# Performance work log

Hardware: AMD Instinct MI355X
Metric: run time of the kernel (lower is better)

## Reference

```python
import jax, jax.numpy as jnp
import numpy as np

B, S, H = 2, 2048, 2048
INTER = 1024
N_ROUTED = 8
ZERO = 4
TOTAL = N_ROUTED + ZERO
TOP_K = 2
SCALE = 1.5


def setup_inputs() -> dict:
    key = jax.random.key(0)
    k0, k1, k2, k3, k4, k5 = jax.random.split(key, 6)
    w = 0.02  # weight init scale
    return {
        "hidden_states": jax.random.normal(k0, (B, S, H), jnp.float32),
        "classifier_w": jax.random.normal(k1, (TOTAL, H), jnp.float32) * w,
        "e_score_correction_bias": jax.random.normal(k2, (TOTAL,), jnp.float32) * w,
        "gate_w": jax.random.normal(k3, (N_ROUTED, INTER, H), jnp.float32) * w,
        "up_w": jax.random.normal(k4, (N_ROUTED, INTER, H), jnp.float32) * w,
        "down_w": jax.random.normal(k5, (N_ROUTED, H, INTER), jnp.float32) * w,
    }


def reference(hidden_states, classifier_w, e_score_correction_bias, gate_w, up_w, down_w):
    x = hidden_states  # [B,S,H]
    total = classifier_w.shape[0]
    n_routed = gate_w.shape[0]

    # --- Router: softmax over all experts, bias only for selection ---
    logits = jnp.einsum('bsh,eh->bse', x, classifier_w)          # [B,S,total]
    probs = jax.nn.softmax(logits, axis=-1)
    biased = probs + e_score_correction_bias
    _, idx = jax.lax.top_k(biased, TOP_K)                         # [B,S,K] int
    rw = jnp.take_along_axis(probs, idx, axis=-1) * SCALE         # unbiased probs as weights

    # Dense per-expert weight via one-hot combine (Equal+Mul+ReduceSum in original)
    w_full = jnp.sum(jax.nn.one_hot(idx, total, dtype=x.dtype) * rw[..., None], axis=-2)  # [B,S,total]

    # --- Compute ALL routed experts densely (matches original op graph) ---
    g = jnp.einsum('bsh,eih->bsei', x, gate_w)                    # [B,S,E,INTER]
    u = jnp.einsum('bsh,eih->bsei', x, up_w)
    act = jax.nn.silu(g) * u
    expert_out = jnp.einsum('bsei,ehi->bseh', act, down_w)        # [B,S,E,H]

    out = jnp.einsum('bse,bseh->bsh', w_full[..., :n_routed], expert_out)
    # Zero (identity) experts pass hidden_states through
    out = out + x * jnp.sum(w_full[..., n_routed:], axis=-1, keepdims=True)
    return out
```

## Files before the change

kernel.cpp:

```cpp
#include <hip/hip_runtime.h>
#include <cstdint>

#define T_TOKENS 4096
#define HDIM 2048
#define IDIM 1024
#define NEXP 8
#define NTOT 12
#define MAX_SLOTS 8320

typedef __bf16 bf16x8_t __attribute__((ext_vector_type(8)));
typedef float f32x4_t __attribute__((ext_vector_type(4)));
typedef unsigned short u16x8_t __attribute__((ext_vector_type(8)));

__device__ __forceinline__ unsigned short f2bf(float f) {
    unsigned int u = __builtin_bit_cast(unsigned int, f);
    u += 0x7fffu + ((u >> 16) & 1u);
    return (unsigned short)(u >> 16);
}
__device__ __forceinline__ float bfu2f(unsigned short u) {
    unsigned int v = ((unsigned int)u) << 16;
    return __builtin_bit_cast(float, v);
}
__device__ __forceinline__ void async16(const unsigned short* g, unsigned short* l) {
    __builtin_amdgcn_global_load_lds(
        (const unsigned int __attribute__((address_space(1)))*)g,
        (unsigned int __attribute__((address_space(3)))*)l,
        16, 0, 0);
}
__device__ __forceinline__ void cvt16(const float* src, unsigned short* dst) {
    f32x4_t f0 = ((const f32x4_t*)src)[0];
    f32x4_t f1 = ((const f32x4_t*)src)[1];
    f32x4_t f2 = ((const f32x4_t*)src)[2];
    f32x4_t f3 = ((const f32x4_t*)src)[3];
    u16x8_t a, b;
#pragma unroll
    for (int j = 0; j < 4; ++j) { a[j] = f2bf(f0[j]); a[4 + j] = f2bf(f1[j]); }
#pragma unroll
    for (int j = 0; j < 4; ++j) { b[j] = f2bf(f2[j]); b[4 + j] = f2bf(f3[j]); }
    ((u16x8_t*)dst)[0] = a;
    ((u16x8_t*)dst)[1] = b;
}

__global__ void init_kernel(int* __restrict__ meta) {
    int i = threadIdx.x;
    if (i < 32) meta[i] = 0;
}

__global__ void noop_kernel() {}

__global__ void router_kernel(const float* __restrict__ x,
                              const float* __restrict__ cw,
                              const float* __restrict__ bias,
                              int* __restrict__ counts,
                              int* __restrict__ tok_e,
                              float* __restrict__ tok_w,
                              float* __restrict__ zero_w) {
    const int token = blockIdx.x;
    const int ln = threadIdx.x;
    const float* xr = x + (size_t)token * HDIM;
    float acc[NTOT];
#pragma unroll
    for (int e = 0; e < NTOT; ++e) acc[e] = 0.f;
    for (int h0 = ln * 4; h0 < HDIM; h0 += 256) {
        f32x4_t xv = *(const f32x4_t*)(xr + h0);
#pragma unroll
        for (int e = 0; e < NTOT; ++e) {
            f32x4_t wv = *(const f32x4_t*)(cw + e * HDIM + h0);
            acc[e] += xv[0] * wv[0] + xv[1] * wv[1] + xv[2] * wv[2] + xv[3] * wv[3];
        }
    }
#pragma unroll
    for (int e = 0; e < NTOT; ++e) {
        float v = acc[e];
#pragma unroll
        for (int s = 32; s > 0; s >>= 1) v += __shfl_xor(v, s, 64);
        acc[e] = v;
    }
    if (ln == 0) {
        float mx = acc[0];
#pragma unroll
        for (int e = 1; e < NTOT; ++e) mx = fmaxf(mx, acc[e]);
        float p[NTOT];
        float sum = 0.f;
#pragma unroll
        for (int e = 0; e < NTOT; ++e) { p[e] = __expf(acc[e] - mx); sum += p[e]; }
        float inv = 1.f / sum;
#pragma unroll
        for (int e = 0; e < NTOT; ++e) p[e] *= inv;
        float b[NTOT];
#pragma unroll
        for (int e = 0; e < NTOT; ++e) b[e] = p[e] + bias[e];
        int i0 = 0; float v0 = b[0];
#pragma unroll
        for (int e = 1; e < NTOT; ++e) if (b[e] > v0) { v0 = b[e]; i0 = e; }
        int i1 = -1; float v1 = -3.0e38f;
#pragma unroll
        for (int e = 0; e < NTOT; ++e) if (e != i0 && b[e] > v1) { v1 = b[e]; i1 = e; }
        if (i1 < 0) i1 = (i0 == 0) ? 1 : 0;
        float w0 = p[i0] * 1.5f, w1 = p[i1] * 1.5f;
        tok_e[2 * token] = i0; tok_e[2 * token + 1] = i1;
        tok_w[2 * token] = w0; tok_w[2 * token + 1] = w1;
        float zw = 0.f;
        if (i0 >= NEXP) zw += w0; else atomicAdd(&counts[i0], 1);
        if (i1 >= NEXP) zw += w1; else atomicAdd(&counts[i1], 1);
        zero_w[token] = zw;
    }
}

__global__ void scan_kernel(const int* __restrict__ counts, int* __restrict__ offs) {
    if (threadIdx.x == 0 && blockIdx.x == 0) {
        int a = 0;
        for (int e = 0; e < NEXP; ++e) {
            offs[e] = a;
            int c = counts[e];
            if (c < 0) c = 0;
            if (c > T_TOKENS) c = T_TOKENS;
            a += c;
        }
        if (a > 2 * T_TOKENS) a = 2 * T_TOKENS;
        offs[NEXP] = a;
    }
}

__global__ void place_kernel(const int* __restrict__ tok_e, const float* __restrict__ tok_w,
                             const int* __restrict__ offs, int* __restrict__ fill,
                             int* __restrict__ token_list, float* __restrict__ slot_w,
                             int* __restrict__ map) {
    int token = blockIdx.x * blockDim.x + threadIdx.x;
    if (token >= T_TOKENS) return;
#pragma unroll
    for (int j = 0; j < 2; ++j) {
        int e = tok_e[2 * token + j];
        int m = -1;
        if (e >= 0 && e < NEXP) {
            int pos = atomicAdd(&fill[e], 1);
            int slot = offs[e] + pos;
            if (slot >= 0 && slot < 2 * T_TOKENS) {
                token_list[slot] = token;
                slot_w[slot] = tok_w[2 * token + j];
                m = slot;
            }
        }
        map[2 * token + j] = m;
    }
}

__launch_bounds__(256, 2)
__global__ void gemm1_kernel(const float* __restrict__ x,
                             const float* __restrict__ gate_w,
                             const float* __restrict__ up_w,
                             const int* __restrict__ offs,
                             const int* __restrict__ token_list,
                             const float* __restrict__ slot_w,
                             unsigned short* __restrict__ act) {
    const int e = blockIdx.z;
    const int off = offs[e];
    int Me = offs[e + 1] - off;
    if (Me < 0) Me = 0;
    if (Me > T_TOKENS) Me = T_TOKENS;
    const int m0 = blockIdx.y * 128;
    if (m0 >= Me) return;
    const int n0 = blockIdx.x * 128;

    __shared__ __align__(16) unsigned short As[128][32];
    __shared__ __align__(16) unsigned short Gs[128][32];
    __shared__ __align__(16) unsigned short Us[128][32];

    const int tid = threadIdx.x;
    const int srow = tid >> 1;
    const int shalf = (tid & 1) * 16;

    int tr = m0 + srow; if (tr >= Me) tr = Me - 1;
    int tok = token_list[off + tr];
    if (tok < 0 || tok >= T_TOKENS) tok = 0;
    const float* aA = x + (size_t)tok * HDIM + shalf;
    const float* aG = gate_w + (size_t)e * IDIM * HDIM + (size_t)(n0 + srow) * HDIM + shalf;
    const float* aU = up_w + (size_t)e * IDIM * HDIM + (size_t)(n0 + srow) * HDIM + shalf;
    unsigned short* lA = &As[srow][shalf];
    unsigned short* lG = &Gs[srow][shalf];
    unsigned short* lU = &Us[srow][shalf];

    const int wv = tid >> 6, ln = tid & 63;
    const int wm = wv & 1, wn = wv >> 1;
    const int fr = ln & 15;
    const int fk = (ln >> 4) * 8;

    f32x4_t accg[4][4] = {};
    f32x4_t accu[4][4] = {};

    for (int k0 = 0; k0 < HDIM; k0 += 32) {
        cvt16(aA + k0, lA);
        cvt16(aG + k0, lG);
        cvt16(aU + k0, lU);
        __syncthreads();
        bf16x8_t af[4], gf[4], uf[4];
#pragma unroll
        for (int t = 0; t < 4; ++t) {
            af[t] = *(const bf16x8_t*)&As[wm * 64 + t * 16 + fr][fk];
            gf[t] = *(const bf16x8_t*)&Gs[wn * 64 + t * 16 + fr][fk];
            uf[t] = *(const bf16x8_t*)&Us[wn * 64 + t * 16 + fr][fk];
        }
#pragma unroll
        for (int mt = 0; mt < 4; ++mt)
#pragma unroll
            for (int nt = 0; nt < 4; ++nt) {
                accg[mt][nt] = __builtin_amdgcn_mfma_f32_16x16x32_bf16(af[mt], gf[nt], accg[mt][nt], 0, 0, 0);
                accu[mt][nt] = __builtin_amdgcn_mfma_f32_16x16x32_bf16(af[mt], uf[nt], accu[mt][nt], 0, 0, 0);
            }
        __syncthreads();
    }

#pragma unroll
    for (int mt = 0; mt < 4; ++mt) {
#pragma unroll
        for (int r = 0; r < 4; ++r) {
            int rloc = wm * 64 + mt * 16 + (ln >> 4) * 4 + r;
            int grow = m0 + rloc;
            if (grow < Me) {
                float w = slot_w[off + grow];
                size_t rb = (size_t)(off + grow) * IDIM + n0;
#pragma unroll
                for (int nt = 0; nt < 4; ++nt) {
                    float g = accg[mt][nt][r];
                    float u = accu[mt][nt][r];
                    float s = g / (1.f + __expf(-g));
                    act[rb + wn * 64 + nt * 16 + fr] = f2bf(s * u * w);
                }
            }
        }
    }
}

__launch_bounds__(256, 2)
__global__ void gemm2_kernel(const unsigned short* __restrict__ act,
                             const float* __restrict__ dwn,
                             const int* __restrict__ offs,
                             unsigned short* __restrict__ dout) {
    const int e = blockIdx.z;
    const int off = offs[e];
    int Me = offs[e + 1] - off;
    if (Me < 0) Me = 0;
    if (Me > T_TOKENS) Me = T_TOKENS;
    const int m0 = blockIdx.y * 128;
    if (m0 >= Me) return;
    const int n0 = blockIdx.x * 128;

    __shared__ __align__(16) unsigned short As[128][32];
    __shared__ __align__(16) unsigned short Bs[128][32];

    const int tid = threadIdx.x;
    const int wv = tid >> 6, ln = tid & 63;

    const int sr0 = wv * 16 + (ln >> 2);
    const int sc = (ln & 3) * 8;
    int ar0 = off + m0 + sr0;      if (ar0 >= MAX_SLOTS) ar0 = MAX_SLOTS - 1;
    int ar1 = off + m0 + 64 + sr0; if (ar1 >= MAX_SLOTS) ar1 = MAX_SLOTS - 1;
    const unsigned short* aA0 = act + (size_t)ar0 * IDIM + sc;
    const unsigned short* aA1 = act + (size_t)ar1 * IDIM + sc;
    unsigned short* lA0 = &As[wv * 16][0];
    unsigned short* lA1 = &As[64 + wv * 16][0];

    const int srow = tid >> 1;
    const int shalf = (tid & 1) * 16;
    const float* aB = dwn + (size_t)e * HDIM * IDIM + (size_t)(n0 + srow) * IDIM + shalf;
    unsigned short* lB = &Bs[srow][shalf];

    const int wm = wv & 1, wn = wv >> 1;
    const int fr = ln & 15;
    const int fk = (ln >> 4) * 8;

    f32x4_t acc[4][4] = {};

    for (int k0 = 0; k0 < IDIM; k0 += 32) {
        async16(aA0 + k0, lA0);
        async16(aA1 + k0, lA1);
        cvt16(aB + k0, lB);
        __syncthreads();
        bf16x8_t af[4], bfr[4];
#pragma unroll
        for (int t = 0; t < 4; ++t) {
            af[t] = *(const bf16x8_t*)&As[wm * 64 + t * 16 + fr][fk];
            bfr[t] = *(const bf16x8_t*)&Bs[wn * 64 + t * 16 + fr][fk];
        }
#pragma unroll
        for (int mt = 0; mt < 4; ++mt)
#pragma unroll
            for (int nt = 0; nt < 4; ++nt)
                acc[mt][nt] = __builtin_amdgcn_mfma_f32_16x16x32_bf16(af[mt], bfr[nt], acc[mt][nt], 0, 0, 0);
        __syncthreads();
    }

#pragma unroll
    for (int mt = 0; mt < 4; ++mt) {
#pragma unroll
        for (int r = 0; r < 4; ++r) {
            int rloc = wm * 64 + mt * 16 + (ln >> 4) * 4 + r;
            int grow = m0 + rloc;
            if (grow < Me) {
                size_t rb = (size_t)(off + grow) * HDIM + n0;
#pragma unroll
                for (int nt = 0; nt < 4; ++nt)
                    dout[rb + wn * 64 + nt * 16 + fr] = f2bf(acc[mt][nt][r]);
            }
        }
    }
}

__global__ void finalize_kernel(const float* __restrict__ x,
                                const unsigned short* __restrict__ dout,
                                const int* __restrict__ map,
                                const float* __restrict__ zero_w,
                                float* __restrict__ out) {
    int gid = blockIdx.x * blockDim.x + threadIdx.x;
    int token = gid >> 8;
    int hg = (gid & 255) * 8;
    int s0 = map[2 * token], s1 = map[2 * token + 1];
    float zw = zero_w[token];
    size_t base = (size_t)token * HDIM + hg;
    f32x4_t x0 = *(const f32x4_t*)(x + base);
    f32x4_t x1 = *(const f32x4_t*)(x + base + 4);
    float o[8];
#pragma unroll
    for (int j = 0; j < 4; ++j) { o[j] = zw * x0[j]; o[4 + j] = zw * x1[j]; }
    if (s0 >= 0 && s0 < 2 * T_TOKENS) {
        u16x8_t d = *(const u16x8_t*)(dout + (size_t)s0 * HDIM + hg);
#pragma unroll
        for (int j = 0; j < 8; ++j) o[j] += bfu2f(d[j]);
    }
    if (s1 >= 0 && s1 < 2 * T_TOKENS) {
        u16x8_t d = *(const u16x8_t*)(dout + (size_t)s1 * HDIM + hg);
#pragma unroll
        for (int j = 0; j < 8; ++j) o[j] += bfu2f(d[j]);
    }
    f32x4_t o0, o1;
#pragma unroll
    for (int j = 0; j < 4; ++j) { o0[j] = o[j]; o1[j] = o[4 + j]; }
    *(f32x4_t*)(out + base) = o0;
    *(f32x4_t*)(out + base + 4) = o1;
}

extern "C" void kernel_launch(void* const* d_in, const int* in_sizes, int n_in,
                              void* d_out, int out_size, void* d_ws, size_t ws_size,
                              hipStream_t stream) {
    const float* x = (const float*)d_in[0];
    const float* cw = (const float*)d_in[1];
    const float* bias = (const float*)d_in[2];
    const float* gw = (const float*)d_in[3];
    const float* uw = (const float*)d_in[4];
    const float* dw = (const float*)d_in[5];
    float* out = (float*)d_out;

    char* ws = (char*)d_ws;
    int* counts = (int*)(ws + 0);
    int* fill = (int*)(ws + 32);
    int* offs = (int*)(ws + 64);
    int* tok_e = (int*)(ws + 128);
    float* tok_w = (float*)(ws + 32896);
    float* zero_w = (float*)(ws + 65664);
    int* map = (int*)(ws + 82048);
    int* token_list = (int*)(ws + 114816);
    float* slot_w = (float*)(ws + 148096);
    unsigned short* act = (unsigned short*)(ws + 181504);
    unsigned short* dout = (unsigned short*)(ws + 181504 + 17039360);
    const size_t needed = 181504ull + 17039360ull + 34078720ull;
    if (ws_size < needed) {
        noop_kernel<<<1, 64, 0, stream>>>();
        return;
    }

    init_kernel<<<1, 64, 0, stream>>>((int*)ws);

    router_kernel<<<T_TOKENS, 64, 0, stream>>>(x, cw, bias, counts, tok_e, tok_w, zero_w);
    scan_kernel<<<1, 64, 0, stream>>>(counts, offs);
    place_kernel<<<(T_TOKENS + 255) / 256, 256, 0, stream>>>(tok_e, tok_w, offs, fill,
                                                             token_list, slot_w, map);
    gemm1_kernel<<<dim3(IDIM / 128, 32, NEXP), 256, 0, stream>>>(x, gw, uw, offs,
                                                                 token_list, slot_w, act);
    gemm2_kernel<<<dim3(HDIM / 128, 32, NEXP), 256, 0, stream>>>(act, dw, offs, dout);
    finalize_kernel<<<(T_TOKENS * HDIM / 8 + 255) / 256, 256, 0, stream>>>(x, dout, map,
                                                                           zero_w, out);
}
```

Baseline: 518.5 us.

## Pre-convert weights and activations to bf16 and use async LDS loads in GEMMs

Adds per-call kernels converting gate/up/down weights to bf16 in workspace and writes a bf16 copy of x from the router. GEMM kernels then load bf16 operands directly into LDS via global_load_lds, with gemm1 using 64-row tiles and higher occupancy. This removes in-loop fp32→bf16 conversion and halves repeated weight traffic, at the cost of an extra ~300MB conversion pass every call. A fallback keeps the old kernels when the workspace is too small.

```diff
diff --git a/kernel.cpp b/kernel.cpp
--- a/kernel.cpp
+++ b/kernel.cpp
@@ -11,6 +11,7 @@
 typedef __bf16 bf16x8_t __attribute__((ext_vector_type(8)));
 typedef float f32x4_t __attribute__((ext_vector_type(4)));
 typedef unsigned short u16x8_t __attribute__((ext_vector_type(8)));
+typedef unsigned short u16x4_t __attribute__((ext_vector_type(4)));
 
 __device__ __forceinline__ unsigned short f2bf(float f) {
     unsigned int u = __builtin_bit_cast(unsigned int, f);
@@ -48,13 +49,26 @@
 
 __global__ void noop_kernel() {}
 
+__global__ void cvtbf_kernel(const float* __restrict__ s, unsigned short* __restrict__ d, int n8) {
+    int stride = gridDim.x * blockDim.x;
+    for (int i = blockIdx.x * blockDim.x + threadIdx.x; i < n8; i += stride) {
+        const f32x4_t* p = (const f32x4_t*)(s + (size_t)i * 8);
+        f32x4_t a = p[0], b = p[1];
+        u16x8_t o;
+#pragma unroll
+        for (int j = 0; j < 4; ++j) { o[j] = f2bf(a[j]); o[4 + j] = f2bf(b[j]); }
+        ((u16x8_t*)d)[i] = o;
+    }
+}
+
 __global__ void router_kernel(const float* __restrict__ x,
                               const float* __restrict__ cw,
                               const float* __restrict__ bias,
                               int* __restrict__ counts,
                               int* __restrict__ tok_e,
                               float* __restrict__ tok_w,
-                              float* __restrict__ zero_w) {
+                              float* __restrict__ zero_w,
+                              unsigned short* __restrict__ xb) {
     const int token = blockIdx.x;
     const int ln = threadIdx.x;
     const float* xr = x + (size_t)token * HDIM;
@@ -63,6 +77,12 @@
     for (int e = 0; e < NTOT; ++e) acc[e] = 0.f;
     for (int h0 = ln * 4; h0 < HDIM; h0 += 256) {
         f32x4_t xv = *(const f32x4_t*)(xr + h0);
+        if (xb) {
+            u16x4_t o;
+#pragma unroll
+            for (int j = 0; j < 4; ++j) o[j] = f2bf(xv[j]);
+            *(u16x4_t*)(xb + (size_t)token * HDIM + h0) = o;
+        }
 #pragma unroll
         for (int e = 0; e < NTOT; ++e) {
             f32x4_t wv = *(const f32x4_t*)(cw + e * HDIM + h0);
@@ -145,10 +165,10 @@
     }
 }
 
-__launch_bounds__(256, 2)
-__global__ void gemm1_kernel(const float* __restrict__ x,
-                             const float* __restrict__ gate_w,
-                             const float* __restrict__ up_w,
+__launch_bounds__(256, 3)
+__global__ void gemm1_kernel(const unsigned short* __restrict__ xb,
+                             const unsigned short* __restrict__ gwb,
+                             const unsigned short* __restrict__ uwb,
                              const int* __restrict__ offs,
                              const int* __restrict__ token_list,
                              const float* __restrict__ slot_w,
@@ -158,6 +178,178 @@
     int Me = offs[e + 1] - off;
     if (Me < 0) Me = 0;
     if (Me > T_TOKENS) Me = T_TOKENS;
+    const int m0 = blockIdx.y * 64;
+    if (m0 >= Me) return;
+    const int n0 = blockIdx.x * 128;
+
+    __shared__ __align__(16) unsigned short As[64][32];
+    __shared__ __align__(16) unsigned short Gs[128][32];
+    __shared__ __align__(16) unsigned short Us[128][32];
+
+    const int tid = threadIdx.x;
+    const int wv = tid >> 6, ln = tid & 63;
+
+    int tr = m0 + wv * 16 + (ln >> 2);
+    if (tr >= Me) tr = Me - 1;
+    int tok = token_list[off + tr];
+    if (tok < 0 || tok >= T_TOKENS) tok = 0;
+    const unsigned short* aA = xb + (size_t)tok * HDIM + (ln & 3) * 8;
+    unsigned short* lA = &As[wv * 16][0];
+
+    const size_t wrow = (size_t)(n0 + wv * 32 + (ln >> 2)) * HDIM + (ln & 3) * 8;
+    const unsigned short* aG0 = gwb + (size_t)e * IDIM * HDIM + wrow;
+    const unsigned short* aG1 = aG0 + (size_t)16 * HDIM;
+    const unsigned short* aU0 = uwb + (size_t)e * IDIM * HDIM + wrow;
+    const unsigned short* aU1 = aU0 + (size_t)16 * HDIM;
+    unsigned short* lG0 = &Gs[wv * 32][0];
+    unsigned short* lG1 = &Gs[wv * 32 + 16][0];
+    unsigned short* lU0 = &Us[wv * 32][0];
+    unsigned short* lU1 = &Us[wv * 32 + 16][0];
+
+    const int wm = wv & 1, wn = wv >> 1;
+    const int fr = ln & 15;
+    const int fk = (ln >> 4) * 8;
+
+    f32x4_t accg[2][4] = {};
+    f32x4_t accu[2][4] = {};
+
+    for (int k0 = 0; k0 < HDIM; k0 += 32) {
+        async16(aA + k0, lA);
+        async16(aG0 + k0, lG0);
+        async16(aG1 + k0, lG1);
+        async16(aU0 + k0, lU0);
+        async16(aU1 + k0, lU1);
+        __syncthreads();
+        bf16x8_t af[2], gf[4], uf[4];
+#pragma unroll
+        for (int t = 0; t < 2; ++t)
+            af[t] = *(const bf16x8_t*)&As[wm * 32 + t * 16 + fr][fk];
+#pragma unroll
+        for (int t = 0; t < 4; ++t) {
+            gf[t] = *(const bf16x8_t*)&Gs[wn * 64 + t * 16 + fr][fk];
+            uf[t] = *(const bf16x8_t*)&Us[wn * 64 + t * 16 + fr][fk];
+        }
+#pragma unroll
+        for (int mt = 0; mt < 2; ++mt)
+#pragma unroll
+            for (int nt = 0; nt < 4; ++nt) {
+                accg[mt][nt] = __builtin_amdgcn_mfma_f32_16x16x32_bf16(af[mt], gf[nt], accg[mt][nt], 0, 0, 0);
+                accu[mt][nt] = __builtin_amdgcn_mfma_f32_16x16x32_bf16(af[mt], uf[nt], accu[mt][nt], 0, 0, 0);
+            }
+        __syncthreads();
+    }
+
+#pragma unroll
+    for (int mt = 0; mt < 2; ++mt) {
+#pragma unroll
+        for (int r = 0; r < 4; ++r) {
+            int rloc = wm * 32 + mt * 16 + (ln >> 4) * 4 + r;
+            int grow = m0 + rloc;
+            if (grow < Me) {
+                float w = slot_w[off + grow];
+                size_t rb = (size_t)(off + grow) * IDIM + n0;
+#pragma unroll
+                for (int nt = 0; nt < 4; ++nt) {
+                    float g = accg[mt][nt][r];
+                    float u = accu[mt][nt][r];
+                    float s = g / (1.f + __expf(-g));
+                    act[rb + wn * 64 + nt * 16 + fr] = f2bf(s * u * w);
+                }
+            }
+        }
+    }
+}
+
+__launch_bounds__(256, 3)
+__global__ void gemm2_kernel(const unsigned short* __restrict__ act,
+                             const unsigned short* __restrict__ dwb,
+                             const int* __restrict__ offs,
+                             unsigned short* __restrict__ dout) {
+    const int e = blockIdx.z;
+    const int off = offs[e];
+    int Me = offs[e + 1] - off;
+    if (Me < 0) Me = 0;
+    if (Me > T_TOKENS) Me = T_TOKENS;
+    const int m0 = blockIdx.y * 128;
+    if (m0 >= Me) return;
+    const int n0 = blockIdx.x * 128;
+
+    __shared__ __align__(16) unsigned short As[128][32];
+    __shared__ __align__(16) unsigned short Bs[128][32];
+
+    const int tid = threadIdx.x;
+    const int wv = tid >> 6, ln = tid & 63;
+    const int sc = (ln & 3) * 8;
+
+    const int sr = wv * 16 + (ln >> 2);
+    int ar0 = off + m0 + sr;      if (ar0 >= MAX_SLOTS) ar0 = MAX_SLOTS - 1;
+    int ar1 = off + m0 + 64 + sr; if (ar1 >= MAX_SLOTS) ar1 = MAX_SLOTS - 1;
+    const unsigned short* aA0 = act + (size_t)ar0 * IDIM + sc;
+    const unsigned short* aA1 = act + (size_t)ar1 * IDIM + sc;
+    unsigned short* lA0 = &As[wv * 16][0];
+    unsigned short* lA1 = &As[64 + wv * 16][0];
+
+    const unsigned short* aB0 = dwb + (size_t)e * HDIM * IDIM +
+                                (size_t)(n0 + wv * 32 + (ln >> 2)) * IDIM + sc;
+    const unsigned short* aB1 = aB0 + (size_t)16 * IDIM;
+    unsigned short* lB0 = &Bs[wv * 32][0];
+    unsigned short* lB1 = &Bs[wv * 32 + 16][0];
+
+    const int wm = wv & 1, wn = wv >> 1;
+    const int fr = ln & 15;
+    const int fk = (ln >> 4) * 8;
+
+    f32x4_t acc[4][4] = {};
+
+    for (int k0 = 0; k0 < IDIM; k0 += 32) {
+        async16(aA0 + k0, lA0);
+        async16(aA1 + k0, lA1);
+        async16(aB0 + k0, lB0);
+        async16(aB1 + k0, lB1);
+        __syncthreads();
+        bf16x8_t af[4], bfr[4];
+#pragma unroll
+        for (int t = 0; t < 4; ++t) {
+            af[t] = *(const bf16x8_t*)&As[wm * 64 + t * 16 + fr][fk];
+            bfr[t] = *(const bf16x8_t*)&Bs[wn * 64 + t * 16 + fr][fk];
+        }
+#pragma unroll
+        for (int mt = 0; mt < 4; ++mt)
+#pragma unroll
+            for (int nt = 0; nt < 4; ++nt)
+                acc[mt][nt] = __builtin_amdgcn_mfma_f32_16x16x32_bf16(af[mt], bfr[nt], acc[mt][nt], 0, 0, 0);
+        __syncthreads();
+    }
+
+#pragma unroll
+    for (int mt = 0; mt < 4; ++mt) {
+#pragma unroll
+        for (int r = 0; r < 4; ++r) {
+            int rloc = wm * 64 + mt * 16 + (ln >> 4) * 4 + r;
+            int grow = m0 + rloc;
+            if (grow < Me) {
+                size_t rb = (size_t)(off + grow) * HDIM + n0;
+#pragma unroll
+                for (int nt = 0; nt < 4; ++nt)
+                    dout[rb + wn * 64 + nt * 16 + fr] = f2bf(acc[mt][nt][r]);
+            }
+        }
+    }
+}
+
+__launch_bounds__(256, 2)
+__global__ void gemm1_fb(const float* __restrict__ x,
+                         const float* __restrict__ gate_w,
+                         const float* __restrict__ up_w,
+                         const int* __restrict__ offs,
+                         const int* __restrict__ token_list,
+                         const float* __restrict__ slot_w,
+                         unsigned short* __restrict__ act) {
+    const int e = blockIdx.z;
+    const int off = offs[e];
+    int Me = offs[e + 1] - off;
+    if (Me < 0) Me = 0;
+    if (Me > T_TOKENS) Me = T_TOKENS;
     const int m0 = blockIdx.y * 128;
     if (m0 >= Me) return;
     const int n0 = blockIdx.x * 128;
@@ -232,10 +424,10 @@
 }
 
 __launch_bounds__(256, 2)
-__global__ void gemm2_kernel(const unsigned short* __restrict__ act,
-                             const float* __restrict__ dwn,
-                             const int* __restrict__ offs,
-                             unsigned short* __restrict__ dout) {
+__global__ void gemm2_fb(const unsigned short* __restrict__ act,
+                         const float* __restrict__ dwn,
+                         const int* __restrict__ offs,
+                         unsigned short* __restrict__ dout) {
     const int e = blockIdx.z;
     const int off = offs[e];
     int Me = offs[e + 1] - off;
@@ -361,22 +553,44 @@
     int* token_list = (int*)(ws + 114816);
     float* slot_w = (float*)(ws + 148096);
     unsigned short* act = (unsigned short*)(ws + 181504);
-    unsigned short* dout = (unsigned short*)(ws + 181504 + 17039360);
-    const size_t needed = 181504ull + 17039360ull + 34078720ull;
-    if (ws_size < needed) {
+    unsigned short* dout = (unsigned short*)(ws + 17220864);
+    const size_t needed_small = 51299584ull;
+    unsigned short* xb  = (unsigned short*)(ws + 51299584ull);
+    unsigned short* gwb = (unsigned short*)(ws + 68076800ull);
+    unsigned short* uwb = (unsigned short*)(ws + 101631232ull);
+    unsigned short* dwb = (unsigned short*)(ws + 135185664ull);
+    const size_t needed_big = 168740096ull;
+
+    if (ws_size < needed_small) {
         noop_kernel<<<1, 64, 0, stream>>>();
         return;
     }
 
     init_kernel<<<1, 64, 0, stream>>>((int*)ws);
 
-    router_kernel<<<T_TOKENS, 64, 0, stream>>>(x, cw, bias, counts, tok_e, tok_w, zero_w);
-    scan_kernel<<<1, 64, 0, stream>>>(counts, offs);
-    place_kernel<<<(T_TOKENS + 255) / 256, 256, 0, stream>>>(tok_e, tok_w, offs, fill,
-                                                             token_list, slot_w, map);
-    gemm1_kernel<<<dim3(IDIM / 128, 32, NEXP), 256, 0, stream>>>(x, gw, uw, offs,
+    if (ws_size >= needed_big) {
+        router_kernel<<<T_TOKENS, 64, 0, stream>>>(x, cw, bias, counts, tok_e, tok_w, zero_w, xb);
+        scan_kernel<<<1, 64, 0, stream>>>(counts, offs);
+        place_kernel<<<(T_TOKENS + 255) / 256, 256, 0, stream>>>(tok_e, tok_w, offs, fill,
+                                                                 token_list, slot_w, map);
+        const int n8w = NEXP * IDIM * HDIM / 8;
+        cvtbf_kernel<<<2048, 256, 0, stream>>>(gw, gwb, n8w);
+        cvtbf_kernel<<<2048, 256, 0, stream>>>(uw, uwb, n8w);
+        cvtbf_kernel<<<2048, 256, 0, stream>>>(dw, dwb, n8w);
+        gemm1_kernel<<<dim3(IDIM / 128, 64, NEXP), 256, 0, stream>>>(xb, gwb, uwb, offs,
+                                                                     token_list, slot_w, act);
+        gemm2_kernel<<<dim3(HDIM / 128, 32, NEXP), 256, 0, stream>>>(act, dwb, offs, dout);
+    } else {
+        router_kernel<<<T_TOKENS, 64, 0, stream>>>(x, cw, bias, counts, tok_e, tok_w, zero_w,
+                                                   (unsigned short*)nullptr);
+        scan_kernel<<<1, 64, 0, stream>>>(counts, offs);
+        place_kernel<<<(T_TOKENS + 255) / 256, 256, 0, stream>>>(tok_e, tok_w, offs, fill,
+                                                                 token_list, slot_w, map);
+        gemm1_fb<<<dim3(IDIM / 128, 32, NEXP), 256, 0, stream>>>(x, gw, uw, offs,
                                                                  token_list, slot_w, act);
-    gemm2_kernel<<<dim3(HDIM / 128, 32, NEXP), 256, 0, stream>>>(act, dw, offs, dout);
+        gemm2_fb<<<dim3(HDIM / 128, 32, NEXP), 256, 0, stream>>>(act, dw, offs, dout);
+    }
+
     finalize_kernel<<<(T_TOKENS * HDIM / 8 + 255) / 256, 256, 0, stream>>>(x, dout, map,
                                                                            zero_w, out);
 }
```

Measured after the change: 531.8 us. +2.6%, slower.
